# Optimization experiments

Hardware: AMD Instinct MI355X
Metric: run time of the kernel (lower is better)

## Reference

```python
import jax, jax.numpy as jnp
import numpy as np

N, E, B = 20000, 60000, 512
F_IN, ED, H, C = 7, 3, 4, 256
HC = H * C  # 1024
D_MODEL = 1024
EPS_BN = 1e-5


def setup_inputs() -> dict:
    key = jax.random.key(0)
    ks = jax.random.split(key, 24)
    s = 0.05
    inp = {
        'x': jax.random.normal(ks[0], (N, F_IN), jnp.float32),
        'edge_index': jax.random.randint(ks[1], (2, E), 0, N, jnp.int32),
        'edge_attr': jax.random.normal(ks[2], (E, ED), jnp.float32),
        'batch': jnp.sort(jax.random.randint(ks[3], (N,), 0, B, jnp.int32)),
        'w0': jax.random.normal(ks[4], (F_IN, HC), jnp.float32) * s,
        'w_rest': jax.random.normal(ks[5], (3, HC, HC), jnp.float32) * s,
        'w_edge': jax.random.normal(ks[6], (4, ED, HC), jnp.float32) * s,
        'att_src': jax.random.normal(ks[7], (4, H, C), jnp.float32) * s,
        'att_dst': jax.random.normal(ks[8], (4, H, C), jnp.float32) * s,
        'att_edge': jax.random.normal(ks[9], (4, H, C), jnp.float32) * s,
        'bias012': jax.random.normal(ks[10], (3, HC), jnp.float32) * s,
        'bias3': jax.random.normal(ks[11], (C,), jnp.float32) * s,
        'bn_gamma': jnp.ones((3, HC), jnp.float32),
        'bn_beta': jnp.zeros((3, HC), jnp.float32),
        'bn_mean': jnp.zeros((3, HC), jnp.float32),
        'bn_var': jnp.ones((3, HC), jnp.float32),
        'gate_w': jax.random.normal(ks[12], (C, 1), jnp.float32) * s,
        'gate_b': jnp.zeros((1,), jnp.float32),
        'proj_w': jax.random.normal(ks[13], (C, D_MODEL), jnp.float32) * s,
        'proj_b': jnp.zeros((D_MODEL,), jnp.float32),
    }
    return inp


def _gat_layer(x, ei, ea, W, We, a_s, a_d, a_e, bias, concat):
    # PyG GATConv with edge_dim, add_self_loops=True (fill_value='mean'), eval mode (no dropout)
    n = x.shape[0]
    sl = jnp.arange(n, dtype=ei.dtype)
    ea_mean = ea.mean(axis=0)
    ei = jnp.concatenate([ei, jnp.stack([sl, sl])], axis=1)            # [2, E+N]
    ea = jnp.concatenate([ea, jnp.broadcast_to(ea_mean, (n, ea.shape[1]))], axis=0)
    h = (x @ W).reshape(n, H, C)                                       # [N,H,C]
    alpha_src = jnp.einsum('nhc,hc->nh', h, a_s)
    alpha_dst = jnp.einsum('nhc,hc->nh', h, a_d)
    eh = (ea @ We).reshape(-1, H, C)
    alpha_e = jnp.einsum('ehc,hc->eh', eh, a_e)
    src, dst = ei[0], ei[1]
    alpha = jax.nn.leaky_relu(alpha_src[src] + alpha_dst[dst] + alpha_e, 0.2)  # [E+N,H]
    amax = jax.ops.segment_max(alpha, dst, num_segments=n)
    alpha = jnp.exp(alpha - amax[dst])
    denom = jax.ops.segment_sum(alpha, dst, num_segments=n)
    alpha = alpha / (denom[dst] + 1e-16)
    msg = h[src] * alpha[:, :, None]                                   # [E+N,H,C]
    out = jax.ops.segment_sum(msg, dst, num_segments=n)                # [N,H,C]
    out = out.reshape(n, H * C) if concat else out.mean(axis=1)
    return out + bias


def reference(x, edge_index, edge_attr, batch, w0, w_rest, w_edge, att_src, att_dst,
              att_edge, bias012, bias3, bn_gamma, bn_beta, bn_mean, bn_var,
              gate_w, gate_b, proj_w, proj_b):
    h = x
    for i in range(4):
        W = w0 if i == 0 else w_rest[i - 1]
        concat = i < 3
        b = bias012[i] if concat else bias3
        h = _gat_layer(h, edge_index, edge_attr, W, w_edge[i],
                       att_src[i], att_dst[i], att_edge[i], b, concat)
        if i < 3:
            # BatchNorm1d in eval mode, then ReLU (dropout is identity in eval)
            h = (h - bn_mean[i]) * (bn_gamma[i] / jnp.sqrt(bn_var[i] + EPS_BN)) + bn_beta[i]
            h = jax.nn.relu(h)
    # AttentionalAggregation: segment softmax over gate scores, weighted sum per graph
    gate = h @ gate_w + gate_b                                         # [N,1]
    gmax = jax.ops.segment_max(gate, batch, num_segments=B)
    g = jnp.exp(gate - gmax[batch])
    gsum = jax.ops.segment_sum(g, batch, num_segments=B)
    w = g / (gsum[batch] + 1e-16)
    graph = jax.ops.segment_sum(w * h, batch, num_segments=B)          # [B,256]
    return graph @ proj_w + proj_b                                     # [B,1024]
```

## Files before the change

kernel.cpp:

```cpp
#include <hip/hip_runtime.h>
#include <math.h>

#define NN 20000
#define NP 20480
#define EE 60000
#define BB 512
#define HC 1024
#define HH 4
#define CC 256

typedef _Float16 f16;
typedef f16 half8 __attribute__((ext_vector_type(8)));
typedef f16 f16x4 __attribute__((ext_vector_type(4)));
typedef float floatx4 __attribute__((ext_vector_type(4)));
typedef float floatx16 __attribute__((ext_vector_type(16)));

__device__ __forceinline__ size_t af_off(int n, int c) {
    int mblk = n >> 7, rr = n & 127;
    int iter = c >> 5, kc = c & 31;
    int kh = kc >> 4, kg = (kc >> 3) & 1, e = kc & 7;
    return ((((size_t)(mblk * 32 + iter) * 2 + kh) * 4 + (rr >> 5)) * 64 +
            (kg * 32 + (rr & 31))) * 8 + e;
}

__device__ __forceinline__ int node_remap(int bid) {
    return (bid >> 3) + (bid & 7) * 2500;
}

__device__ __forceinline__ void gload16(const f16* g, f16* l) {
    __builtin_amdgcn_global_load_lds((const __attribute__((address_space(1))) void*)g,
                                     (__attribute__((address_space(3))) void*)l, 16, 0, 0);
}

__global__ void ehist_kernel(const float* __restrict__ ea, const int* __restrict__ ei,
                             float* sums, int* counts, int E_) {
    int e = blockIdx.x * 256 + threadIdx.x;
    float s0 = 0.f, s1 = 0.f, s2 = 0.f;
    if (e < E_) {
        atomicAdd(&counts[ei[E_ + e]], 1);
        s0 = ea[e * 3 + 0];
        s1 = ea[e * 3 + 1];
        s2 = ea[e * 3 + 2];
    }
    for (int o = 32; o; o >>= 1) {
        s0 += __shfl_down(s0, o);
        s1 += __shfl_down(s1, o);
        s2 += __shfl_down(s2, o);
    }
    if ((threadIdx.x & 63) == 0) {
        atomicAdd(&sums[0], s0);
        atomicAdd(&sums[1], s1);
        atomicAdd(&sums[2], s2);
    }
}

__global__ void scan1_kernel(const int* __restrict__ counts, int* __restrict__ partial,
                             int* __restrict__ psums, int n) {
    __shared__ int sdata[256];
    int t = threadIdx.x;
    int i = blockIdx.x * 256 + t;
    int v = (i < n) ? counts[i] : 0;
    sdata[t] = v;
    __syncthreads();
#pragma unroll
    for (int off = 1; off < 256; off <<= 1) {
        int tmp = (t >= off) ? sdata[t - off] : 0;
        __syncthreads();
        sdata[t] += tmp;
        __syncthreads();
    }
    if (i < n) partial[i] = sdata[t];
    if (t == 255) psums[blockIdx.x] = sdata[255];
}

__global__ void scan2_kernel(int* __restrict__ psums, int nb) {
    __shared__ int sdata[128];
    int t = threadIdx.x;
    sdata[t] = (t < nb) ? psums[t] : 0;
    __syncthreads();
#pragma unroll
    for (int off = 1; off < 128; off <<= 1) {
        int tmp = (t >= off) ? sdata[t - off] : 0;
        __syncthreads();
        sdata[t] += tmp;
        __syncthreads();
    }
    if (t < nb) psums[t] = (t == 0) ? 0 : sdata[t - 1];
}

__global__ void scan3_kernel(const int* __restrict__ partial, const int* __restrict__ psums,
                             int* __restrict__ indptr, int n) {
    int i = blockIdx.x * 256 + threadIdx.x;
    if (i == 0) indptr[0] = 0;
    if (i < n) indptr[i + 1] = partial[i] + psums[blockIdx.x];
}

__global__ void scatter_kernel(const int* __restrict__ ei, const int* __restrict__ indptr,
                               int* fill, int* sorted, int* sdst, int E_) {
    int e = blockIdx.x * 256 + threadIdx.x;
    if (e >= E_) return;
    int d = ei[E_ + e];
    int pos = indptr[d] + atomicAdd(&fill[d], 1);
    sorted[pos] = e;
    sdst[pos] = d;
}

__global__ void bptr_kernel(const int* __restrict__ batch, int* bptr, int n, int nb) {
    int i = blockIdx.x * 256 + threadIdx.x;
    if (i >= n) return;
    int b = batch[i];
    if (i == 0) {
        for (int bb = 0; bb <= b; bb++) bptr[bb] = 0;
    } else {
        int pb = batch[i - 1];
        if (pb != b) {
            for (int bb = pb + 1; bb <= b; bb++) bptr[bb] = i;
        }
    }
    if (i == n - 1) {
        for (int bb = b + 1; bb <= nb; bb++) bptr[bb] = n;
    }
}

__global__ void prep0_kernel(const float* __restrict__ w_rest, f16* __restrict__ Bf,
                             const float* __restrict__ att_src,
                             const float* __restrict__ att_dst,
                             const float* __restrict__ w0,
                             const float* __restrict__ bias012, const float* __restrict__ bn_g,
                             const float* __restrict__ bn_b, const float* __restrict__ bn_m,
                             const float* __restrict__ bn_v,
                             const float* __restrict__ w_edge,
                             const float* __restrict__ att_edge,
                             const float* __restrict__ ea_sums,
                             float* __restrict__ wsv, float* __restrict__ wdv,
                             float* __restrict__ w0s, float* __restrict__ w0d,
                             float2* __restrict__ bnss,
                             float* __restrict__ Mmat, float* __restrict__ ae_self,
                             float invE) {
    int bid = blockIdx.x;
    int t = threadIdx.x;
    if (bid < 768) {
        __shared__ float tile[64][65];
        int bx = (bid & 15) * 64;
        int by = ((bid >> 4) & 15) * 64;
        int l = bid >> 8;
        int tr = t >> 6, tc = t & 63;
#pragma unroll
        for (int i = 0; i < 16; i++) {
            int r = by + i * 4 + tr;
            tile[i * 4 + tr][tc] = w_rest[(size_t)l * 1048576 + (size_t)r * 1024 + bx + tc];
        }
        __syncthreads();
        f16* bl = Bf + (size_t)l * 1048576;
#pragma unroll
        for (int ii = 0; ii < 2; ii++) {
            int idx = ii * 256 + t;
            int nl = idx >> 3, kg8 = idx & 7;
            int n = bx + nl, k = by + kg8 * 8;
            half8 v;
#pragma unroll
            for (int e = 0; e < 8; e++) v[e] = (f16)tile[kg8 * 8 + e][nl];
            *(half8*)&bl[af_off(n, k)] = v;
        }
    } else if (bid < 3840) {
        int b = bid - 768;
        int l = b >> 10, k = b & 1023;
        int hp = t >> 6, lane = t & 63;
        int col = hp * 256 + lane * 4;
        const float* wrow = w_rest + (size_t)l * 1048576 + (size_t)k * 1024;
        float4 w4 = *(const float4*)&wrow[col];
        float4 a4 = *(const float4*)&att_src[(l + 1) * HC + col];
        float4 d4 = *(const float4*)&att_dst[(l + 1) * HC + col];
        float sp = w4.x * a4.x + w4.y * a4.y + w4.z * a4.z + w4.w * a4.w;
        float dp = w4.x * d4.x + w4.y * d4.y + w4.z * d4.z + w4.w * d4.w;
        for (int m = 1; m < 64; m <<= 1) {
            sp += __shfl_xor(sp, m);
            dp += __shfl_xor(dp, m);
        }
        if (lane == 0) {
            wsv[((size_t)l * 1024 + k) * 4 + hp] = sp;
            wdv[((size_t)l * 1024 + k) * 4 + hp] = dp;
        }
    } else if (bid < 3847) {
        int f = bid - 3840;
        int hp = t >> 6, lane = t & 63;
        int col = hp * 256 + lane * 4;
        float4 w4 = *(const float4*)&w0[f * HC + col];
        float4 a4 = *(const float4*)&att_src[col];
        float4 d4 = *(const float4*)&att_dst[col];
        float sp = w4.x * a4.x + w4.y * a4.y + w4.z * a4.z + w4.w * a4.w;
        float dp = w4.x * d4.x + w4.y * d4.y + w4.z * d4.z + w4.w * d4.w;
        for (int m = 1; m < 64; m <<= 1) {
            sp += __shfl_xor(sp, m);
            dp += __shfl_xor(dp, m);
        }
        if (lane == 0) {
            w0s[f * 4 + hp] = sp;
            w0d[f * 4 + hp] = dp;
        }
    } else if (bid < 3859) {
        int i = (bid - 3847) * 256 + t;
        if (i < 3 * HC) {
            float s = bn_g[i] * rsqrtf(bn_v[i] + 1e-5f);
            float2 o;
            o.x = s;
            o.y = (bias012[i] - bn_m[i]) * s + bn_b[i];
            bnss[i] = o;
        }
    } else {
        __shared__ float red[256];
        __shared__ float Ms[12];
        int l = bid - 3859;
        for (int dh = 0; dh < 12; dh++) {
            int d = dh >> 2, hh = dh & 3;
            float v = w_edge[l * 3072 + d * HC + hh * CC + t] *
                      att_edge[l * HC + hh * CC + t];
            red[t] = v;
            __syncthreads();
            for (int o = 128; o; o >>= 1) {
                if (t < o) red[t] += red[t + o];
                __syncthreads();
            }
            if (t == 0) {
                Ms[dh] = red[0];
                Mmat[l * 12 + dh] = red[0];
            }
            __syncthreads();
        }
        if (t < 4) {
            float v = 0.f;
            for (int d = 0; d < 3; d++) v += ea_sums[d] * invE * Ms[d * 4 + t];
            ae_self[l * 4 + t] = v;
        }
    }
}

__global__ void prep2_kernel(const int* __restrict__ ei, const int* __restrict__ sorted,
                             const float* __restrict__ ea, const float* __restrict__ Mmat,
                             int* __restrict__ ssrc, float* __restrict__ aeh_pk,
                             const float* __restrict__ x, const float* __restrict__ w0s,
                             const float* __restrict__ w0d, float* __restrict__ asrc,
                             float* __restrict__ adst, float* __restrict__ xpad) {
    int bid = blockIdx.x;
    int t = threadIdx.x;
    if (bid < 235) {
        int idx = bid * 256 + t;
        if (idx >= EE) return;
        int eid = sorted[idx];
        ssrc[idx] = ei[eid];
        float a0 = ea[eid * 3 + 0], a1 = ea[eid * 3 + 1], a2 = ea[eid * 3 + 2];
#pragma unroll
        for (int l = 0; l < 4; l++) {
#pragma unroll
            for (int h = 0; h < 4; h++) {
                aeh_pk[(size_t)idx * 16 + l * 4 + h] =
                    a0 * Mmat[l * 12 + h] + a1 * Mmat[l * 12 + 4 + h] +
                    a2 * Mmat[l * 12 + 8 + h];
            }
        }
    } else {
        int n = (bid - 235) * 256 + t;
        if (n >= NN) return;
        float xr[7];
#pragma unroll
        for (int f = 0; f < 7; f++) xr[f] = x[n * 7 + f];
        float4 p0, p1;
        p0.x = xr[0]; p0.y = xr[1]; p0.z = xr[2]; p0.w = xr[3];
        p1.x = xr[4]; p1.y = xr[5]; p1.z = xr[6]; p1.w = 0.f;
        *(float4*)&xpad[(size_t)n * 8] = p0;
        *(float4*)&xpad[(size_t)n * 8 + 4] = p1;
#pragma unroll
        for (int hp = 0; hp < 4; hp++) {
            float s = 0.f, d = 0.f;
#pragma unroll
            for (int f = 0; f < 7; f++) {
                s += xr[f] * w0s[f * 4 + hp];
                d += xr[f] * w0d[f * 4 + hp];
            }
            asrc[n * 4 + hp] = s;
            adst[n * 4 + hp] = d;
        }
    }
}

__global__ void edgep_kernel(const int* __restrict__ ssrc, const int* __restrict__ sdst,
                             const float* __restrict__ aeh_pk, const float* __restrict__ asrc,
                             const float* __restrict__ adst, float* __restrict__ pe,
                             int layer) {
    int i = blockIdx.x * 256 + threadIdx.x;
    if (i >= EE) return;
    int src = ssrc[i];
    int dst = sdst[i];
    float4 a = *(const float4*)&asrc[(size_t)src * 4];
    float4 d = *(const float4*)&adst[(size_t)dst * 4];
    float4 m = *(const float4*)&aeh_pk[(size_t)i * 16 + layer * 4];
    float r[4] = {a.x + d.x + m.x, a.y + d.y + m.y, a.z + d.z + m.z, a.w + d.w + m.w};
    float4 o;
#pragma unroll
    for (int k = 0; k < 4; k++) {
        float v = (r[k] > 0.f) ? r[k] : 0.2f * r[k];
        (&o.x)[k] = __expf(v);
    }
    *(float4*)&pe[(size_t)i * 4] = o;
}

__global__ void agg0x_kernel(const float* __restrict__ xpad, const float* __restrict__ asrc,
                             const float* __restrict__ adst, const float* __restrict__ ae_self,
                             const int* __restrict__ ssrc, const float* __restrict__ pe,
                             const int* __restrict__ indptr, float* __restrict__ xagg) {
    int n = blockIdx.x * 256 + threadIdx.x;
    if (n >= NN) return;
    float4 as4 = *(const float4*)&asrc[(size_t)n * 4];
    float4 ad4 = *(const float4*)&adst[(size_t)n * 4];
    float adl[4] = {ad4.x, ad4.y, ad4.z, ad4.w};
    float asl[4] = {as4.x, as4.y, as4.z, as4.w};
    float4 x0 = *(const float4*)&xpad[(size_t)n * 8];
    float4 x1 = *(const float4*)&xpad[(size_t)n * 8 + 4];
    float xr[7] = {x0.x, x0.y, x0.z, x0.w, x1.x, x1.y, x1.z};
    float denom[4];
    float xa[4][7];
#pragma unroll
    for (int h = 0; h < 4; h++) {
        float r = asl[h] + adl[h] + ae_self[h];
        r = (r > 0.f) ? r : 0.2f * r;
        float p = __expf(r);
        denom[h] = p;
#pragma unroll
        for (int f = 0; f < 7; f++) xa[h][f] = p * xr[f];
    }
    int s = indptr[n], e = indptr[n + 1];
    for (int idx = s; idx < e; idx++) {
        int src = ssrc[idx];
        float4 pv = *(const float4*)&pe[(size_t)idx * 4];
        float pl[4] = {pv.x, pv.y, pv.z, pv.w};
        float4 s0 = *(const float4*)&xpad[(size_t)src * 8];
        float4 s1 = *(const float4*)&xpad[(size_t)src * 8 + 4];
        float xs[7] = {s0.x, s0.y, s0.z, s0.w, s1.x, s1.y, s1.z};
#pragma unroll
        for (int h = 0; h < 4; h++) {
            denom[h] += pl[h];
#pragma unroll
            for (int f = 0; f < 7; f++) xa[h][f] += pl[h] * xs[f];
        }
    }
#pragma unroll
    for (int h = 0; h < 4; h++) {
        float inv = 1.0f / (denom[h] + 1e-16f);
#pragma unroll
        for (int f = 0; f < 7; f++) xagg[(size_t)n * 28 + h * 7 + f] = xa[h][f] * inv;
    }
}

__global__ void gemm7f_kernel(const float* __restrict__ xagg, const float* __restrict__ w0,
                              const float2* __restrict__ bnss, const float* __restrict__ wsv,
                              const float* __restrict__ wdv, f16* __restrict__ outAf,
                              float* __restrict__ asrc_n, float* __restrict__ adst_n) {
    __shared__ float xs[32][29];
    __shared__ float red[4][32][8];
    int bid = blockIdx.x;
    int t = threadIdx.x;
    int n0 = bid * 32;
    int mblk = bid >> 2, rg = bid & 3;
    for (int i = t; i < 896; i += 256) xs[i / 28][i % 28] = xagg[(size_t)n0 * 28 + i];
    __syncthreads();
    int w = t >> 6, lane = t & 63;
    int lr = lane & 31, kg = lane >> 5;
    float x7[7];
#pragma unroll
    for (int f = 0; f < 7; f++) x7[f] = xs[lr][w * 7 + f];
    float sp[4] = {0.f, 0.f, 0.f, 0.f}, dp[4] = {0.f, 0.f, 0.f, 0.f};
#pragma unroll
    for (int p = 0; p < 16; p++) {
        int iter = w * 8 + (p >> 1);
        int kh = p & 1;
        int c0 = iter * 32 + (kh * 2 + kg) * 8;
        float dot[8];
#pragma unroll
        for (int e = 0; e < 8; e++) dot[e] = 0.f;
#pragma unroll
        for (int f = 0; f < 7; f++) {
            float4 wa = *(const float4*)&w0[f * HC + c0];
            float4 wb = *(const float4*)&w0[f * HC + c0 + 4];
            dot[0] += x7[f] * wa.x; dot[1] += x7[f] * wa.y;
            dot[2] += x7[f] * wa.z; dot[3] += x7[f] * wa.w;
            dot[4] += x7[f] * wb.x; dot[5] += x7[f] * wb.y;
            dot[6] += x7[f] * wb.z; dot[7] += x7[f] * wb.w;
        }
        half8 o;
#pragma unroll
        for (int e = 0; e < 8; e++) {
            int j = c0 + e;
            float2 ss = bnss[j];
            float val = fmaxf(fmaf(dot[e], ss.x, ss.y), 0.f);
            o[e] = (f16)val;
            float4 w4s = *(const float4*)&wsv[(size_t)j * 4];
            float4 w4d = *(const float4*)&wdv[(size_t)j * 4];
            sp[0] += val * w4s.x; sp[1] += val * w4s.y;
            sp[2] += val * w4s.z; sp[3] += val * w4s.w;
            dp[0] += val * w4d.x; dp[1] += val * w4d.y;
            dp[2] += val * w4d.z; dp[3] += val * w4d.w;
        }
        size_t off = ((((size_t)(mblk * 32 + iter) * 2 + kh) * 4 + rg) * 64 + lane) * 8;
        *(half8*)&outAf[off] = o;
    }
#pragma unroll
    for (int q = 0; q < 4; q++) {
        sp[q] += __shfl_xor(sp[q], 32);
        dp[q] += __shfl_xor(dp[q], 32);
    }
    if (kg == 0) {
#pragma unroll
        for (int q = 0; q < 4; q++) {
            red[w][lr][q] = sp[q];
            red[w][lr][4 + q] = dp[q];
        }
    }
    __syncthreads();
    {
        int lr2 = t >> 3, q = t & 7;
        float v = red[0][lr2][q] + red[1][lr2][q] + red[2][lr2][q] + red[3][lr2][q];
        if (q < 4) asrc_n[(size_t)(n0 + lr2) * 4 + q] = v;
        else adst_n[(size_t)(n0 + lr2) * 4 + (q - 4)] = v;
    }
}

#define EPB 235
__global__ __launch_bounds__(256) void gemmep_kernel(
    const f16* __restrict__ Af, const f16* __restrict__ Bf, f16* __restrict__ C16,
    const int* __restrict__ ssrc, const int* __restrict__ sdst,
    const float* __restrict__ aeh_pk, const float* __restrict__ asrc,
    const float* __restrict__ adst, float* __restrict__ pe, int layer) {
    __shared__ __align__(16) f16 lds[16384];
    int t = threadIdx.x;
    int bid = blockIdx.x;
    if (bid < EPB) {
        int i = bid * 256 + t;
        if (i >= EE) return;
        int src = ssrc[i];
        int dst = sdst[i];
        float4 a = *(const float4*)&asrc[(size_t)src * 4];
        float4 d = *(const float4*)&adst[(size_t)dst * 4];
        float4 m = *(const float4*)&aeh_pk[(size_t)i * 16 + layer * 4];
        float r[4] = {a.x + d.x + m.x, a.y + d.y + m.y, a.z + d.z + m.z, a.w + d.w + m.w};
        float4 o;
#pragma unroll
        for (int k = 0; k < 4; k++) {
            float v = (r[k] > 0.f) ? r[k] : 0.2f * r[k];
            (&o.x)[k] = __expf(v);
        }
        *(float4*)&pe[(size_t)i * 4] = o;
        return;
    }
    int gid = bid - EPB;
    int w = t >> 6, lane = t & 63;
    int g = gid >> 6, rblk = gid & 63;
    int nblk = rblk >> 3;
    int mblk = g * 8 + (rblk & 7);
    int rg0 = (w >> 1) * 2;
    int cg0 = (w & 1) * 2;

    floatx16 acc[2][2];
#pragma unroll
    for (int i = 0; i < 2; i++)
#pragma unroll
        for (int j = 0; j < 2; j++) acc[i][j] = (floatx16)(0.f);

    const f16* ga0 = Af + (size_t)mblk * 131072 + w * 1024 + lane * 8;
    const f16* gb0 = Bf + (size_t)nblk * 131072 + w * 1024 + lane * 8;

    auto STAGE = [&](int it, int b) {
        const f16* ga = ga0 + (size_t)it * 4096;
        const f16* gb = gb0 + (size_t)it * 4096;
        f16* la = &lds[b * 8192 + w * 1024 + lane * 8];
        f16* lb = &lds[b * 8192 + 4096 + w * 1024 + lane * 8];
        gload16(ga, la);
        gload16(ga + 512, la + 512);
        gload16(gb, lb);
        gload16(gb + 512, lb + 512);
    };
    auto COMPUTE = [&](int b) {
        half8 afr[2][2], bfr[2][2];
#pragma unroll
        for (int kh = 0; kh < 2; kh++) {
#pragma unroll
            for (int i = 0; i < 2; i++) {
                afr[kh][i] = *(const half8*)&lds[b * 8192 + kh * 2048 + (rg0 + i) * 512 +
                                                 lane * 8];
                bfr[kh][i] = *(const half8*)&lds[b * 8192 + 4096 + kh * 2048 +
                                                 (cg0 + i) * 512 + lane * 8];
            }
        }
#pragma unroll
        for (int kh = 0; kh < 2; kh++)
#pragma unroll
            for (int i = 0; i < 2; i++)
#pragma unroll
                for (int j = 0; j < 2; j++)
                    acc[i][j] = __builtin_amdgcn_mfma_f32_32x32x16_f16(bfr[kh][j], afr[kh][i],
                                                                       acc[i][j], 0, 0, 0);
    };

    STAGE(0, 0);
    __syncthreads();
#pragma unroll 1
    for (int k2 = 0; k2 < 16; k2++) {
        int i0 = k2 * 2;
        STAGE(i0 + 1, 1);
        COMPUTE(0);
        __syncthreads();
        if (i0 + 2 < 32) STAGE(i0 + 2, 0);
        COMPUTE(1);
        __syncthreads();
    }

    int fr32 = lane & 31, kg = lane >> 5;
#pragma unroll
    for (int i = 0; i < 2; i++) {
        int row = mblk * 128 + rg0 * 32 + i * 32 + fr32;
#pragma unroll
        for (int j = 0; j < 2; j++) {
#pragma unroll
            for (int gq = 0; gq < 4; gq++) {
                f16x4 o;
#pragma unroll
                for (int r = 0; r < 4; r++) o[r] = (f16)acc[i][j][gq * 4 + r];
                *(f16x4*)&C16[(size_t)row * HC + nblk * 128 + cg0 * 32 + j * 32 + gq * 8 +
                              kg * 4] = o;
            }
        }
    }
}

__global__ void agg_kernel(const f16* __restrict__ h16, const float* __restrict__ asrc,
                           const float* __restrict__ adst, const float* __restrict__ ae_self,
                           const int* __restrict__ ssrc, const float* __restrict__ pe,
                           const int* __restrict__ indptr, const float2* __restrict__ bnss,
                           const float* __restrict__ wsv, const float* __restrict__ wdv,
                           const float* __restrict__ bias3, const float* __restrict__ gw,
                           const float* __restrict__ gb, f16* __restrict__ out16,
                           float* __restrict__ asrc_n, float* __restrict__ adst_n,
                           float* __restrict__ out3, float* __restrict__ gate,
                           int layer, int concat) {
    __shared__ float buf[1024];
    __shared__ float red[32];
    int n = node_remap(blockIdx.x);
    int t = threadIdx.x;
    int h = t >> 6, lane = t & 63;
    int c4 = t * 4;

    float r = asrc[n * 4 + h] + adst[n * 4 + h] + ae_self[layer * 4 + h];
    r = (r > 0.f) ? r : 0.2f * r;
    float p = __expf(r);
    float denom = p;
    float ax, ay, az, aw;
    {
        f16x4 v = *(const f16x4*)&h16[(size_t)n * HC + c4];
        ax = p * (float)v[0]; ay = p * (float)v[1];
        az = p * (float)v[2]; aw = p * (float)v[3];
    }
    int s = indptr[n], epos = indptr[n + 1];
    for (int base = s; base < epos; base += 4) {
        int rem = epos - base;
        int src[4];
        float pv[4];
#pragma unroll
        for (int j = 0; j < 4; j++) {
            if (j < rem) {
                src[j] = ssrc[base + j];
                pv[j] = pe[(size_t)(base + j) * 4 + h];
            } else {
                src[j] = n;
                pv[j] = 0.f;
            }
        }
        f16x4 u[4];
#pragma unroll
        for (int j = 0; j < 4; j++) u[j] = *(const f16x4*)&h16[(size_t)src[j] * HC + c4];
#pragma unroll
        for (int j = 0; j < 4; j++) {
            denom += pv[j];
            ax += pv[j] * (float)u[j][0];
            ay += pv[j] * (float)u[j][1];
            az += pv[j] * (float)u[j][2];
            aw += pv[j] * (float)u[j][3];
        }
    }
    float inv = 1.0f / (denom + 1e-16f);
    ax *= inv; ay *= inv; az *= inv; aw *= inv;

    if (concat) {
        float vals[4] = {ax, ay, az, aw};
        f16x4 o;
        float sp[4] = {0.f, 0.f, 0.f, 0.f}, dp[4] = {0.f, 0.f, 0.f, 0.f};
#pragma unroll
        for (int k = 0; k < 4; k++) {
            int j = c4 + k;
            float2 ss = bnss[j];
            float val = fmaxf(fmaf(vals[k], ss.x, ss.y), 0.f);
            o[k] = (f16)val;
            float4 w4s = *(const float4*)&wsv[(size_t)j * 4];
            float4 w4d = *(const float4*)&wdv[(size_t)j * 4];
            sp[0] += val * w4s.x; sp[1] += val * w4s.y;
            sp[2] += val * w4s.z; sp[3] += val * w4s.w;
            dp[0] += val * w4d.x; dp[1] += val * w4d.y;
            dp[2] += val * w4d.z; dp[3] += val * w4d.w;
        }
        *(f16x4*)&out16[af_off(n, c4)] = o;
#pragma unroll
        for (int m = 1; m < 64; m <<= 1) {
#pragma unroll
            for (int j = 0; j < 4; j++) {
                sp[j] += __shfl_xor(sp[j], m);
                dp[j] += __shfl_xor(dp[j], m);
            }
        }
        if (lane == 0) {
#pragma unroll
            for (int j = 0; j < 4; j++) {
                red[h * 8 + j] = sp[j];
                red[h * 8 + 4 + j] = dp[j];
            }
        }
        __syncthreads();
        if (t < 8) {
            float v = red[t] + red[8 + t] + red[16 + t] + red[24 + t];
            if (t < 4) asrc_n[n * 4 + t] = v;
            else adst_n[n * 4 + (t - 4)] = v;
        }
    } else {
        buf[c4 + 0] = ax;
        buf[c4 + 1] = ay;
        buf[c4 + 2] = az;
        buf[c4 + 3] = aw;
        __syncthreads();
        if (t < 64) {
            float gpart = 0.f;
#pragma unroll
            for (int k = 0; k < 4; k++) {
                int c = t * 4 + k;
                float v2 = 0.25f * (buf[c] + buf[256 + c] + buf[512 + c] + buf[768 + c]) +
                           bias3[c];
                out3[(size_t)n * CC + c] = v2;
                gpart += v2 * gw[c];
            }
            for (int o = 32; o; o >>= 1) gpart += __shfl_down(gpart, o);
            if (t == 0) gate[n] = gpart + gb[0];
        }
    }
}

__global__ void graphagg_kernel(const float* __restrict__ gate, const float* __restrict__ h3,
                                const int* __restrict__ bptr, float* __restrict__ graph) {
    __shared__ float red[256];
    __shared__ float wn[256];
    int b = blockIdx.x, t = threadIdx.x;
    int s = bptr[b], epos = bptr[b + 1];
    float m = -3.4e38f;
    for (int n = s + t; n < epos; n += 256) m = fmaxf(m, gate[n]);
    red[t] = m;
    __syncthreads();
    for (int o = 128; o; o >>= 1) {
        if (t < o) red[t] = fmaxf(red[t], red[t + o]);
        __syncthreads();
    }
    float mval = red[0];
    __syncthreads();
    float sum = 0.f;
    for (int n = s + t; n < epos; n += 256) sum += __expf(gate[n] - mval);
    red[t] = sum;
    __syncthreads();
    for (int o = 128; o; o >>= 1) {
        if (t < o) red[t] += red[t + o];
        __syncthreads();
    }
    float ssum = red[0];
    __syncthreads();
    float acc = 0.f;
    for (int base = s; base < epos; base += 256) {
        int n = base + t;
        wn[t] = (n < epos) ? __expf(gate[n] - mval) : 0.f;
        __syncthreads();
        int cnt = min(256, epos - base);
        for (int j = 0; j < cnt; j++) acc += wn[j] * h3[(size_t)(base + j) * CC + t];
        __syncthreads();
    }
    graph[b * CC + t] = acc / (ssum + 1e-16f);
}

__global__ void proj_kernel(const float* __restrict__ graph, const float* __restrict__ pw,
                            const float* __restrict__ pb, float* __restrict__ out) {
    __shared__ float g[8][256];
    int b = blockIdx.x, t = threadIdx.x;
#pragma unroll
    for (int r = 0; r < 8; r++) g[r][t] = graph[(size_t)(b * 8 + r) * 256 + t];
    __syncthreads();
    float acc[8][4];
#pragma unroll
    for (int r = 0; r < 8; r++)
#pragma unroll
        for (int q = 0; q < 4; q++) acc[r][q] = pb[t + q * 256];
    for (int c = 0; c < 256; c++) {
        float w[4];
#pragma unroll
        for (int q = 0; q < 4; q++) w[q] = pw[(size_t)c * 1024 + t + q * 256];
#pragma unroll
        for (int r = 0; r < 8; r++) {
            float gv = g[r][c];
#pragma unroll
            for (int q = 0; q < 4; q++) acc[r][q] += gv * w[q];
        }
    }
#pragma unroll
    for (int r = 0; r < 8; r++)
#pragma unroll
        for (int q = 0; q < 4; q++)
            out[(size_t)(b * 8 + r) * 1024 + t + q * 256] = acc[r][q];
}

extern "C" void kernel_launch(void* const* d_in, const int* in_sizes, int n_in,
                              void* d_out, int out_size, void* d_ws, size_t ws_size,
                              hipStream_t stream) {
    const float* x = (const float*)d_in[0];
    const int* ei = (const int*)d_in[1];
    const float* ea = (const float*)d_in[2];
    const int* batch = (const int*)d_in[3];
    const float* w0 = (const float*)d_in[4];
    const float* w_rest = (const float*)d_in[5];
    const float* w_edge = (const float*)d_in[6];
    const float* att_src = (const float*)d_in[7];
    const float* att_dst = (const float*)d_in[8];
    const float* att_edge = (const float*)d_in[9];
    const float* bias012 = (const float*)d_in[10];
    const float* bias3 = (const float*)d_in[11];
    const float* bn_g = (const float*)d_in[12];
    const float* bn_b = (const float*)d_in[13];
    const float* bn_m = (const float*)d_in[14];
    const float* bn_v = (const float*)d_in[15];
    const float* gate_w = (const float*)d_in[16];
    const float* gate_b = (const float*)d_in[17];
    const float* proj_w = (const float*)d_in[18];
    const float* proj_b = (const float*)d_in[19];
    float* out = (float*)d_out;

    float* ws = (float*)d_ws;
    size_t off = 0;
    f16* h_lin = (f16*)(ws + off); off += (size_t)NP * HC / 2;
    f16* h_af = (f16*)(ws + off); off += (size_t)NP * HC / 2;
    float* h3 = ws + off; off += (size_t)NN * CC;
    f16* Bf = (f16*)(ws + off); off += (size_t)3 * HC * HC / 2;
    float* xpad = ws + off; off += (size_t)NN * 8;
    float* asrcA = ws + off; off += (size_t)NN * 4;
    float* adstA = ws + off; off += (size_t)NN * 4;
    float* asrcB = ws + off; off += (size_t)NN * 4;
    float* adstB = ws + off; off += (size_t)NN * 4;
    float* wsv = ws + off; off += (size_t)3 * HC * 4;
    float* wdv = ws + off; off += (size_t)3 * HC * 4;
    float* w0s = ws + off; off += 28;
    float* w0d = ws + off; off += 28;
    float2* bnss = (float2*)(ws + off); off += (size_t)3 * HC * 2;
    float* aeh_pk = ws + off; off += (size_t)EE * 16;
    float* pbuf = ws + off; off += (size_t)EE * 4;
    float* xagg = ws + off; off += (size_t)NN * 28;
    float* gate = ws + off; off += (size_t)NN;
    float* graph = ws + off; off += (size_t)BB * CC;
    float* ea_sums = ws + off; off += 4;
    float* Mmat = ws + off; off += 48;
    float* ae_self = ws + off; off += 16;
    int* counts = (int*)(ws + off); off += NN;
    int* partial = (int*)(ws + off); off += NN;
    int* psums = (int*)(ws + off); off += 128;
    int* indptr = (int*)(ws + off); off += NN + 1;
    int* fill = (int*)(ws + off); off += NN;
    int* sorted = (int*)(ws + off); off += EE;
    int* ssrc = (int*)(ws + off); off += EE;
    int* sdst = (int*)(ws + off); off += EE;
    int* bptr = (int*)(ws + off); off += BB + 1;

    hipMemsetAsync(ea_sums, 0, 4 * sizeof(float), stream);
    hipMemsetAsync(counts, 0, NN * sizeof(int), stream);
    hipMemsetAsync(fill, 0, NN * sizeof(int), stream);

    ehist_kernel<<<(EE + 255) / 256, 256, 0, stream>>>(ea, ei, ea_sums, counts, EE);
    int nblk = (NN + 255) / 256;
    scan1_kernel<<<nblk, 256, 0, stream>>>(counts, partial, psums, NN);
    scan2_kernel<<<1, 128, 0, stream>>>(psums, nblk);
    scan3_kernel<<<nblk, 256, 0, stream>>>(partial, psums, indptr, NN);
    scatter_kernel<<<(EE + 255) / 256, 256, 0, stream>>>(ei, indptr, fill, sorted, sdst, EE);
    bptr_kernel<<<(NN + 255) / 256, 256, 0, stream>>>(batch, bptr, NN, BB);
    prep0_kernel<<<3863, 256, 0, stream>>>(w_rest, Bf, att_src, att_dst, w0, bias012, bn_g,
                                           bn_b, bn_m, bn_v, w_edge, att_edge, ea_sums,
                                           wsv, wdv, w0s, w0d, bnss, Mmat, ae_self,
                                           1.0f / EE);
    prep2_kernel<<<235 + nblk, 256, 0, stream>>>(ei, sorted, ea, Mmat, ssrc, aeh_pk,
                                                 x, w0s, w0d, asrcA, adstA, xpad);

    edgep_kernel<<<(EE + 255) / 256, 256, 0, stream>>>(ssrc, sdst, aeh_pk, asrcA, adstA,
                                                       pbuf, 0);
    agg0x_kernel<<<nblk, 256, 0, stream>>>(xpad, asrcA, adstA, ae_self, ssrc,
                                           pbuf, indptr, xagg);
    gemm7f_kernel<<<NN / 32, 256, 0, stream>>>(xagg, w0, bnss, wsv, wdv, h_af, asrcB,
                                               adstB);

    float* asrc_cur = asrcB;
    float* adst_cur = adstB;
    float* asrc_nxt = asrcA;
    float* adst_nxt = adstA;
    for (int i = 1; i < 4; i++) {
        gemmep_kernel<<<EPB + (NP / 128) * (HC / 128), 256, 0, stream>>>(
            h_af, Bf + (size_t)(i - 1) * HC * HC, h_lin,
            ssrc, sdst, aeh_pk, asrc_cur, adst_cur, pbuf, i);
        agg_kernel<<<NN, 256, 0, stream>>>(
            h_lin, asrc_cur, adst_cur, ae_self, ssrc, pbuf, indptr, bnss + (size_t)i * HC,
            wsv + (size_t)i * HC * 4, wdv + (size_t)i * HC * 4, bias3, gate_w, gate_b,
            h_af, asrc_nxt, adst_nxt, h3, gate, i, (i < 3) ? 1 : 0);
        float* tmp = asrc_cur; asrc_cur = asrc_nxt; asrc_nxt = tmp;
        tmp = adst_cur; adst_cur = adst_nxt; adst_nxt = tmp;
    }

    graphagg_kernel<<<BB, 256, 0, stream>>>(gate, h3, bptr, graph);
    proj_kernel<<<BB / 8, 256, 0, stream>>>(graph, proj_w, proj_b, out);
}
```

Measured before the change: 623.7 us.

## Deepen GEMM pipeline to two 64-wide K stages with explicit vmcnt waits

Doubles the LDS staging buffer so each stage holds two K-iterations, cutting the loop from 32 to 16 iterations (8 double-iterations). It keeps two stages in flight, replaces __syncthreads with manual s_waitcnt vmcnt plus s_barrier, and raises wave priority around MFMA compute. The aim is to hide global-to-LDS load latency and reduce barrier overhead. The cost is 64KB of LDS per block, which may lower occupancy, and fragile hand-written wait counts.

Measured after the change: 603.9 us. 3.2% less time.

```diff
diff --git a/kernel.cpp b/kernel.cpp
--- a/kernel.cpp
+++ b/kernel.cpp
@@ -430,7 +430,7 @@
     const int* __restrict__ ssrc, const int* __restrict__ sdst,
     const float* __restrict__ aeh_pk, const float* __restrict__ asrc,
     const float* __restrict__ adst, float* __restrict__ pe, int layer) {
-    __shared__ __align__(16) f16 lds[16384];
+    __shared__ __align__(16) f16 lds[32768];
     int t = threadIdx.x;
     int bid = blockIdx.x;
     if (bid < EPB) {
@@ -468,25 +468,24 @@
     const f16* ga0 = Af + (size_t)mblk * 131072 + w * 1024 + lane * 8;
     const f16* gb0 = Bf + (size_t)nblk * 131072 + w * 1024 + lane * 8;
 
-    auto STAGE = [&](int it, int b) {
-        const f16* ga = ga0 + (size_t)it * 4096;
-        const f16* gb = gb0 + (size_t)it * 4096;
-        f16* la = &lds[b * 8192 + w * 1024 + lane * 8];
-        f16* lb = &lds[b * 8192 + 4096 + w * 1024 + lane * 8];
-        gload16(ga, la);
-        gload16(ga + 512, la + 512);
-        gload16(gb, lb);
-        gload16(gb + 512, lb + 512);
+    auto STAGE = [&](int tt, int b) {
+        const f16* ga = ga0 + (size_t)tt * 8192;
+        const f16* gb = gb0 + (size_t)tt * 8192;
+        f16* base = &lds[b * 16384 + w * 1024 + lane * 8];
+        gload16(ga, base);                gload16(ga + 512, base + 512);
+        gload16(ga + 4096, base + 4096);  gload16(ga + 4608, base + 4608);
+        gload16(gb, base + 8192);         gload16(gb + 512, base + 8704);
+        gload16(gb + 4096, base + 12288); gload16(gb + 4608, base + 12800);
     };
-    auto COMPUTE = [&](int b) {
+    auto COMPUTE = [&](int b, int p) {
         half8 afr[2][2], bfr[2][2];
 #pragma unroll
         for (int kh = 0; kh < 2; kh++) {
 #pragma unroll
             for (int i = 0; i < 2; i++) {
-                afr[kh][i] = *(const half8*)&lds[b * 8192 + kh * 2048 + (rg0 + i) * 512 +
-                                                 lane * 8];
-                bfr[kh][i] = *(const half8*)&lds[b * 8192 + 4096 + kh * 2048 +
+                afr[kh][i] = *(const half8*)&lds[b * 16384 + p * 4096 + kh * 2048 +
+                                                 (rg0 + i) * 512 + lane * 8];
+                bfr[kh][i] = *(const half8*)&lds[b * 16384 + 8192 + p * 4096 + kh * 2048 +
                                                  (cg0 + i) * 512 + lane * 8];
             }
         }
@@ -501,16 +500,33 @@
     };
 
     STAGE(0, 0);
-    __syncthreads();
+    STAGE(1, 1);
 #pragma unroll 1
-    for (int k2 = 0; k2 < 16; k2++) {
-        int i0 = k2 * 2;
-        STAGE(i0 + 1, 1);
-        COMPUTE(0);
-        __syncthreads();
-        if (i0 + 2 < 32) STAGE(i0 + 2, 0);
-        COMPUTE(1);
-        __syncthreads();
+    for (int k2 = 0; k2 < 8; k2++) {
+        asm volatile("s_waitcnt vmcnt(8)" ::: "memory");
+        __builtin_amdgcn_s_barrier();
+        __builtin_amdgcn_sched_barrier(0);
+        __builtin_amdgcn_s_setprio(1);
+        COMPUTE(0, 0);
+        COMPUTE(0, 1);
+        __builtin_amdgcn_s_setprio(0);
+        __builtin_amdgcn_s_barrier();
+        __builtin_amdgcn_sched_barrier(0);
+        if (k2 < 7) STAGE(2 * k2 + 2, 0);
+        if (k2 < 7) {
+            asm volatile("s_waitcnt vmcnt(8)" ::: "memory");
+        } else {
+            asm volatile("s_waitcnt vmcnt(0)" ::: "memory");
+        }
+        __builtin_amdgcn_s_barrier();
+        __builtin_amdgcn_sched_barrier(0);
+        __builtin_amdgcn_s_setprio(1);
+        COMPUTE(1, 0);
+        COMPUTE(1, 1);
+        __builtin_amdgcn_s_setprio(0);
+        __builtin_amdgcn_s_barrier();
+        __builtin_amdgcn_sched_barrier(0);
+        if (k2 < 7) STAGE(2 * k2 + 3, 1);
     }
 
     int fr32 = lane & 31, kg = lane >> 5;
```
